# Optimization experiments

Measured on AMD Instinct MI355X. Metric: run time of the kernel, lower is better.

## Reference

```python
import jax, jax.numpy as jnp
import numpy as np

N_HEADS = 32
N_KV_HEADS = 8
HEAD_DIM = 128
ROPE_THETA = 10000.0


def _rope(x, position_ids):
    # x: [B, n_heads, T, hd], position_ids: [B, T]
    hd = x.shape[-1]
    inv_freq = 1.0 / (ROPE_THETA ** (jnp.arange(0, hd, 2, dtype=jnp.float32) / hd))  # [hd/2]
    ang = position_ids.astype(jnp.float32)[:, :, None] * inv_freq[None, None, :]  # [B, T, hd/2]
    emb = jnp.concatenate([ang, ang], axis=-1)  # [B, T, hd] (HF layout)
    cos = jnp.cos(emb)[:, None, :, :]
    sin = jnp.sin(emb)[:, None, :, :]
    x1, x2 = x[..., : hd // 2], x[..., hd // 2 :]
    rot = jnp.concatenate([-x2, x1], axis=-1)
    return x * cos + rot * sin


def setup_inputs() -> dict:
    key = jax.random.key(0)
    ks = jax.random.split(key, 9)
    B, T, D = 16, 1, 4096
    PAST = 4095
    S = PAST + T
    w = 0.02
    return {
        "hidden_states": jax.random.normal(ks[0], (B, T, D), jnp.float32),
        "attention_mask": jnp.zeros((B, 1, T, S), jnp.float32),  # additive mask, all visible
        "position_ids": jnp.full((B, T), PAST, dtype=jnp.int64),
        "past_key": jax.random.normal(ks[1], (B, N_KV_HEADS, PAST, HEAD_DIM), jnp.float32),
        "past_value": jax.random.normal(ks[2], (B, N_KV_HEADS, PAST, HEAD_DIM), jnp.float32),
        "Wq": jax.random.normal(ks[3], (N_HEADS * HEAD_DIM, D), jnp.float32) * w,
        "Wk": jax.random.normal(ks[4], (N_KV_HEADS * HEAD_DIM, D), jnp.float32) * w,
        "Wv": jax.random.normal(ks[5], (N_KV_HEADS * HEAD_DIM, D), jnp.float32) * w,
        "Wo": jax.random.normal(ks[6], (D, N_HEADS * HEAD_DIM), jnp.float32) * w,
    }


def reference(hidden_states, attention_mask, position_ids, past_key, past_value, Wq, Wk, Wv, Wo):
    B, T, D = hidden_states.shape
    hd = HEAD_DIM
    # q/k/v projections (Llama: no bias)
    q = jnp.einsum("btd,ed->bte", hidden_states, Wq).reshape(B, T, N_HEADS, hd).transpose(0, 2, 1, 3)
    k_new = jnp.einsum("btd,ed->bte", hidden_states, Wk).reshape(B, T, N_KV_HEADS, hd).transpose(0, 2, 1, 3)
    v_new = jnp.einsum("btd,ed->bte", hidden_states, Wv).reshape(B, T, N_KV_HEADS, hd).transpose(0, 2, 1, 3)
    # RoPE on the new token(s); past cache entries are already rotated
    q = _rope(q, position_ids)
    k_new = _rope(k_new, position_ids)
    # static-cache update: write new K/V at position past_seq_len (append)
    k_cache = jnp.concatenate([past_key, k_new], axis=2)   # [B, n_kv, S, hd]
    v_cache = jnp.concatenate([past_value, v_new], axis=2)
    # GQA: repeat kv heads
    n_rep = N_HEADS // N_KV_HEADS
    k = jnp.repeat(k_cache, n_rep, axis=1)  # [B, H, S, hd]
    v = jnp.repeat(v_cache, n_rep, axis=1)
    scores = jnp.einsum("bhtd,bhsd->bhts", q, k) / jnp.sqrt(jnp.float32(hd))
    scores = scores + attention_mask  # additive mask [B,1,T,S]
    w_attn = jax.nn.softmax(scores, axis=-1)
    ctx = jnp.einsum("bhts,bhsd->bhtd", w_attn, v)  # [B, H, T, hd]
    ctx = ctx.transpose(0, 2, 1, 3).reshape(B, T, N_HEADS * hd)
    attn_output = jnp.einsum("bte,de->btd", ctx, Wo)
    return attn_output, k_cache, v_cache
```

## Files before the change

### kernel.cpp

```cpp
#include <hip/hip_runtime.h>

#define NB 16
#define DMODEL 4096
#define NH 32
#define NKV 8
#define HD 128
#define SEQ 4096
#define PASTN 4095
#define EQKV 6144
#define NCHUNK 16
#define CHUNKS 256
#define PSTRIDE 136
#define SCALE 0.08838834764831845f

typedef float v4f __attribute__((ext_vector_type(4)));

__global__ __launch_bounds__(256) void qkv_proj(
    const float* __restrict__ hs, const float* __restrict__ Wq,
    const float* __restrict__ Wk, const float* __restrict__ Wv,
    float* __restrict__ raw ) {
  __shared__ __align__(16) float smem[4 * 32 * 33];
  const int tid = threadIdx.x, wid = tid >> 6, lane = tid & 63;
  const int e0 = blockIdx.x * 8 + wid * 2;

  const float* wrow[2];
#pragma unroll
  for (int r = 0; r < 2; ++r) {
    int e = e0 + r;
    wrow[r] = (e < 4096) ? (Wq + (size_t)e * DMODEL)
            : (e < 5120) ? (Wk + (size_t)(e - 4096) * DMODEL)
                         : (Wv + (size_t)(e - 5120) * DMODEL);
  }

  float acc[2][16];
#pragma unroll
  for (int r = 0; r < 2; ++r)
#pragma unroll
    for (int b = 0; b < 16; ++b) acc[r][b] = 0.f;

  float* ld = smem;
  for (int k0 = 0; k0 < DMODEL; k0 += 256) {
    __syncthreads();
#pragma unroll
    for (int i = 0; i < 4; ++i) {
      int flat = i * 1024 + tid * 4;
      int bb = flat >> 8, c = flat & 255;
      *(v4f*)(&ld[bb * 256 + c]) = *(const v4f*)(hs + (size_t)bb * DMODEL + k0 + c);
    }
    __syncthreads();
    v4f w4[2];
#pragma unroll
    for (int r = 0; r < 2; ++r) w4[r] = *(const v4f*)(wrow[r] + k0 + lane * 4);
#pragma unroll
    for (int b = 0; b < 16; ++b) {
      v4f h4 = *(const v4f*)(&ld[b * 256 + lane * 4]);
#pragma unroll
      for (int r = 0; r < 2; ++r) {
        v4f t = w4[r] * h4;
        acc[r][b] += t[0] + t[1] + t[2] + t[3];
      }
    }
  }

#pragma unroll
  for (int r = 0; r < 2; ++r)
#pragma unroll
    for (int b = 0; b < 16; ++b) acc[r][b] += __shfl_xor(acc[r][b], 32);

  __syncthreads();
  if (lane < 32) {
#pragma unroll
    for (int r = 0; r < 2; ++r)
#pragma unroll
      for (int b = 0; b < 16; ++b)
        smem[(wid * 32 + lane) * 33 + r * 16 + b] = acc[r][b];
  }
  __syncthreads();
  if (lane < 32) {
    float s = 0.f;
#pragma unroll
    for (int t2 = 0; t2 < 32; ++t2) s += smem[(wid * 32 + t2) * 33 + lane];
    const int r = lane >> 4, bb = lane & 15;
    raw[(size_t)bb * EQKV + e0 + r] = s;
  }
}

__device__ __forceinline__ float rope_val(const float* src, int d, float pos) {
  int i = d & 63;
  float inv_freq = powf(10000.f, -(float)(2 * i) * (1.f / 128.f));
  float ang = pos * inv_freq;
  float s, c;
  sincosf(ang, &s, &c);
  float x = src[d];
  float rot = (d < 64) ? -src[d + 64] : src[d - 64];
  return x * c + rot * s;
}

__global__ void rope_scatter(const float* __restrict__ raw,
                             const void* __restrict__ pos_ids,
                             float* __restrict__ qout,
                             float* __restrict__ kc, float* __restrict__ vc) {
  const int b = blockIdx.y, j = blockIdx.x, d = threadIdx.x;
  const int* pi = (const int*)pos_ids;
  long long pos = (pi[1] == 0 && pi[0] != 0) ? ((const long long*)pos_ids)[b]
                                             : (long long)pi[b];
  const float fpos = (float)pos;
  if (j < 32) {
    const float* src = raw + (size_t)b * EQKV + j * HD;
    qout[(size_t)b * (NH * HD) + j * HD + d] = rope_val(src, d, fpos);
  } else if (j < 40) {
    int kvh = j - 32;
    const float* src = raw + (size_t)b * EQKV + 4096 + kvh * HD;
    kc[(((size_t)b * NKV + kvh) * SEQ + PASTN) * HD + d] = rope_val(src, d, fpos);
  } else {
    int kvh = j - 40;
    vc[(((size_t)b * NKV + kvh) * SEQ + PASTN) * HD + d] =
        raw[(size_t)b * EQKV + 5120 + kvh * HD + d];
  }
}

__global__ __launch_bounds__(256, 4) void attn_decode(
    const float* __restrict__ pastK, const float* __restrict__ pastV,
    const float* __restrict__ qv, const float* __restrict__ mask,
    float* __restrict__ kc, float* __restrict__ vc,
    float* __restrict__ part ) {
  __shared__ __align__(16) float sm[4][4][132];

  const int chunk = blockIdx.x, kv = blockIdx.y, b = blockIdx.z;
  const int tid = threadIdx.x, wid = tid >> 6, lane = tid & 63;
  const int half = lane >> 5, q32 = lane & 31;
  const int fo = q32 * 4;

  v4f q[4];
  const float* qb = qv + (size_t)b * (NH * HD) + kv * 4 * HD + fo;
#pragma unroll
  for (int h = 0; h < 4; ++h) q[h] = *(const v4f*)(qb + h * HD);

  const size_t prow = ((size_t)b * NKV + kv) * PASTN;
  const size_t crow = ((size_t)b * NKV + kv) * SEQ;
  const int base = chunk * CHUNKS + wid * (CHUNKS / 4);
  const float* mrow = mask + (size_t)b * SEQ;

  const float mreg = mrow[base + 2 * q32 + half];

  float m[4], l[4];
  v4f c[4];
#pragma unroll
  for (int h = 0; h < 4; ++h) {
    m[h] = -1e30f; l[h] = 0.f;
    c[h] = (v4f){0.f, 0.f, 0.f, 0.f};
  }

  v4f kq[4], vq[4];
#pragma unroll
  for (int i = 0; i < 4; ++i) {
    const int s = base + 2 * i + half;
    const float* kp = (s < PASTN) ? pastK + (prow + s) * HD + fo
                                  : kc + (crow + s) * HD + fo;
    const float* vp = (s < PASTN) ? pastV + (prow + s) * HD + fo
                                  : vc + (crow + s) * HD + fo;
    kq[i] = __builtin_nontemporal_load((const v4f*)kp);
    vq[i] = __builtin_nontemporal_load((const v4f*)vp);
  }

#pragma unroll 4
  for (int t = 0; t < 32; ++t) {
    const int sp = base + 2 * t;
    const int s = sp + half;
    const v4f kch = kq[t & 3], vch = vq[t & 3];
    if (t < 28) {
      const int s2 = sp + 8 + half;
      const float* kp = (s2 < PASTN) ? pastK + (prow + s2) * HD + fo
                                     : kc + (crow + s2) * HD + fo;
      const float* vp = (s2 < PASTN) ? pastV + (prow + s2) * HD + fo
                                     : vc + (crow + s2) * HD + fo;
      kq[t & 3] = __builtin_nontemporal_load((const v4f*)kp);
      vq[t & 3] = __builtin_nontemporal_load((const v4f*)vp);
    }
    if (s < PASTN) {
      __builtin_nontemporal_store(kch, (v4f*)(kc + (crow + s) * HD + fo));
      __builtin_nontemporal_store(vch, (v4f*)(vc + (crow + s) * HD + fo));
    }

    const float mval = __shfl(mreg, t | (lane & 32));

    float d4[4];
#pragma unroll
    for (int h = 0; h < 4; ++h) {
      v4f tv = q[h] * kch;
      d4[h] = tv[0] + tv[1] + tv[2] + tv[3];
    }
#pragma unroll
    for (int off = 1; off <= 16; off <<= 1)
#pragma unroll
      for (int h = 0; h < 4; ++h) d4[h] += __shfl_xor(d4[h], off);

#pragma unroll
    for (int h = 0; h < 4; ++h) {
      float sc = d4[h] * SCALE + mval;
      if (sc > m[h]) {
        float alpha = __expf(m[h] - sc);
        l[h] *= alpha;
        c[h] *= alpha;
        m[h] = sc;
      }
      float p = __expf(sc - m[h]);
      l[h] += p;
      c[h] += p * vch;
    }
  }

#pragma unroll
  for (int h = 0; h < 4; ++h) {
    float mo = __shfl_xor(m[h], 32);
    float mn = fmaxf(m[h], mo);
    float f = __expf(m[h] - mn);
    l[h] *= f;
    c[h] *= f;
    l[h] += __shfl_xor(l[h], 32);
#pragma unroll
    for (int j = 0; j < 4; ++j) c[h][j] += __shfl_xor(c[h][j], 32);
    m[h] = mn;
  }

  if (half == 0) {
#pragma unroll
    for (int h = 0; h < 4; ++h) {
      if (q32 == 0) { sm[wid][h][0] = m[h]; sm[wid][h][1] = l[h]; }
      *(v4f*)(&sm[wid][h][4 + fo]) = c[h];
    }
  }
  __syncthreads();

  float mstar = -1e30f;
#pragma unroll
  for (int sl = 0; sl < 4; ++sl) mstar = fmaxf(mstar, sm[sl][wid][0]);
  float den = 0.f;
  const int d2 = lane * 2;
  float nx = 0.f, ny = 0.f;
#pragma unroll
  for (int sl = 0; sl < 4; ++sl) {
    float w = __expf(sm[sl][wid][0] - mstar);
    den += w * sm[sl][wid][1];
    nx += w * sm[sl][wid][4 + d2];
    ny += w * sm[sl][wid][4 + d2 + 1];
  }
  float* pp = part + (((size_t)b * NH + kv * 4 + wid) * NCHUNK + chunk) * PSTRIDE;
  if (lane == 0) { pp[0] = mstar; pp[1] = den; }
  float2 nv = {nx, ny};
  *(float2*)(pp + 4 + d2) = nv;
}

__global__ void combine(const float* __restrict__ part, float* __restrict__ ctx) {
  const int bh = blockIdx.x;
  const int lane = threadIdx.x;
  const float* pp = part + (size_t)bh * NCHUNK * PSTRIDE;
  float mstar = -1e30f;
#pragma unroll
  for (int c = 0; c < NCHUNK; ++c) mstar = fmaxf(mstar, pp[c * PSTRIDE]);
  float den = 0.f, nx = 0.f, ny = 0.f;
  const int d2 = lane * 2;
#pragma unroll
  for (int c = 0; c < NCHUNK; ++c) {
    float w = __expf(pp[c * PSTRIDE] - mstar);
    den += w * pp[c * PSTRIDE + 1];
    float2 pv = *(const float2*)(pp + c * PSTRIDE + 4 + d2);
    nx += w * pv.x;
    ny += w * pv.y;
  }
  float inv = 1.0f / den;
  ctx[(size_t)bh * HD + d2] = nx * inv;
  ctx[(size_t)bh * HD + d2 + 1] = ny * inv;
}

__global__ __launch_bounds__(256) void out_proj(
    const float* __restrict__ ctx, const float* __restrict__ Wo,
    float* __restrict__ out) {
  __shared__ __align__(16) float smem[4 * 32 * 33];
  const int tid = threadIdx.x, wid = tid >> 6, lane = tid & 63;
  const int e0 = blockIdx.x * 8 + wid * 2;

  float acc[2][16];
#pragma unroll
  for (int r = 0; r < 2; ++r)
#pragma unroll
    for (int b = 0; b < 16; ++b) acc[r][b] = 0.f;

  float* ld = smem;
  for (int k0 = 0; k0 < DMODEL; k0 += 256) {
    __syncthreads();
#pragma unroll
    for (int i = 0; i < 4; ++i) {
      int flat = i * 1024 + tid * 4;
      int bb = flat >> 8, c = flat & 255;
      *(v4f*)(&ld[bb * 256 + c]) = *(const v4f*)(ctx + (size_t)bb * DMODEL + k0 + c);
    }
    __syncthreads();
    v4f w4[2];
#pragma unroll
    for (int r = 0; r < 2; ++r)
      w4[r] = *(const v4f*)(Wo + (size_t)(e0 + r) * DMODEL + k0 + lane * 4);
#pragma unroll
    for (int b = 0; b < 16; ++b) {
      v4f h4 = *(const v4f*)(&ld[b * 256 + lane * 4]);
#pragma unroll
      for (int r = 0; r < 2; ++r) {
        v4f t = w4[r] * h4;
        acc[r][b] += t[0] + t[1] + t[2] + t[3];
      }
    }
  }

#pragma unroll
  for (int r = 0; r < 2; ++r)
#pragma unroll
    for (int b = 0; b < 16; ++b) acc[r][b] += __shfl_xor(acc[r][b], 32);

  __syncthreads();
  if (lane < 32) {
#pragma unroll
    for (int r = 0; r < 2; ++r)
#pragma unroll
      for (int b = 0; b < 16; ++b)
        smem[(wid * 32 + lane) * 33 + r * 16 + b] = acc[r][b];
  }
  __syncthreads();
  if (lane < 32) {
    float s = 0.f;
#pragma unroll
    for (int t2 = 0; t2 < 32; ++t2) s += smem[(wid * 32 + t2) * 33 + lane];
    const int r = lane >> 4, bb = lane & 15;
    out[(size_t)bb * DMODEL + e0 + r] = s;
  }
}

extern "C" void kernel_launch(void* const* d_in, const int* in_sizes, int n_in,
                              void* d_out, int out_size, void* d_ws, size_t ws_size,
                              hipStream_t stream) {
  const float* hs    = (const float*)d_in[0];
  const float* mask  = (const float*)d_in[1];
  const void*  pos   = d_in[2];
  const float* pastK = (const float*)d_in[3];
  const float* pastV = (const float*)d_in[4];
  const float* Wq    = (const float*)d_in[5];
  const float* Wk    = (const float*)d_in[6];
  const float* Wv    = (const float*)d_in[7];
  const float* Wo    = (const float*)d_in[8];

  float* out  = (float*)d_out;
  float* attn = out;
  float* kc   = out + (size_t)NB * DMODEL;
  float* vc   = kc + (size_t)NB * NKV * SEQ * HD;

  float* ws      = (float*)d_ws;
  float* ws_q    = ws;
  float* ws_raw  = ws_q + (size_t)NB * NH * HD;
  float* ws_part = ws_raw + (size_t)NB * EQKV;
  float* ws_ctx  = ws_part + (size_t)NB * NH * NCHUNK * PSTRIDE;

  qkv_proj<<<EQKV / 8, 256, 0, stream>>>(hs, Wq, Wk, Wv, ws_raw);
  rope_scatter<<<dim3(48, NB), 128, 0, stream>>>(ws_raw, pos, ws_q, kc, vc);
  attn_decode<<<dim3(NCHUNK, NKV, NB), 256, 0, stream>>>(pastK, pastV, ws_q, mask,
                                                         kc, vc, ws_part);
  combine<<<NB * NH, 64, 0, stream>>>(ws_part, ws_ctx);
  out_proj<<<DMODEL / 8, 256, 0, stream>>>(ws_ctx, Wo, attn);
}
```

Before: 289.4 us.

## Double-buffer activation and weight loads in QKV and output projection GEMVs

Both projection kernels now use two LDS buffers for the activation tile. The next chunk's activations and weight vectors are prefetched into registers while the current chunk is being computed. This gives one barrier per iteration instead of two and hides global-load latency behind the FMA work. The cost is more LDS per block (32KB plus the reduction buffer) and more registers, which may reduce occupancy.

```diff
diff --git a/kernel.cpp b/kernel.cpp
--- a/kernel.cpp
+++ b/kernel.cpp
@@ -19,9 +19,11 @@
     const float* __restrict__ hs, const float* __restrict__ Wq,
     const float* __restrict__ Wk, const float* __restrict__ Wv,
     float* __restrict__ raw ) {
-  __shared__ __align__(16) float smem[4 * 32 * 33];
+  __shared__ __align__(16) float ld[2][16][256];
+  __shared__ __align__(16) float red[4][32][33];
   const int tid = threadIdx.x, wid = tid >> 6, lane = tid & 63;
   const int e0 = blockIdx.x * 8 + wid * 2;
+  const int fo = lane * 4;
 
   const float* wrow[2];
 #pragma unroll
@@ -38,28 +40,46 @@
 #pragma unroll
     for (int b = 0; b < 16; ++b) acc[r][b] = 0.f;
 
-  float* ld = smem;
-  for (int k0 = 0; k0 < DMODEL; k0 += 256) {
-    __syncthreads();
-#pragma unroll
-    for (int i = 0; i < 4; ++i) {
-      int flat = i * 1024 + tid * 4;
-      int bb = flat >> 8, c = flat & 255;
-      *(v4f*)(&ld[bb * 256 + c]) = *(const v4f*)(hs + (size_t)bb * DMODEL + k0 + c);
-    }
-    __syncthreads();
-    v4f w4[2];
-#pragma unroll
-    for (int r = 0; r < 2; ++r) w4[r] = *(const v4f*)(wrow[r] + k0 + lane * 4);
+  v4f st[4];
+#pragma unroll
+  for (int i = 0; i < 4; ++i)
+    st[i] = *(const v4f*)(hs + (size_t)(i * 4 + wid) * DMODEL + fo);
+#pragma unroll
+  for (int i = 0; i < 4; ++i)
+    *(v4f*)(&ld[0][i * 4 + wid][fo]) = st[i];
+  v4f w4[2];
+#pragma unroll
+  for (int r = 0; r < 2; ++r) w4[r] = *(const v4f*)(wrow[r] + fo);
+  __syncthreads();
+
+  for (int c = 0; c < 16; ++c) {
+    const int k1 = (c + 1) * 256;
+    v4f w4n[2];
+    if (c < 15) {
+#pragma unroll
+      for (int i = 0; i < 4; ++i)
+        st[i] = *(const v4f*)(hs + (size_t)(i * 4 + wid) * DMODEL + k1 + fo);
+#pragma unroll
+      for (int r = 0; r < 2; ++r) w4n[r] = *(const v4f*)(wrow[r] + k1 + fo);
+    }
+    const float* lb = &ld[c & 1][0][0];
 #pragma unroll
     for (int b = 0; b < 16; ++b) {
-      v4f h4 = *(const v4f*)(&ld[b * 256 + lane * 4]);
+      v4f h4 = *(const v4f*)(lb + b * 256 + fo);
 #pragma unroll
       for (int r = 0; r < 2; ++r) {
         v4f t = w4[r] * h4;
         acc[r][b] += t[0] + t[1] + t[2] + t[3];
       }
     }
+    if (c < 15) {
+#pragma unroll
+      for (int i = 0; i < 4; ++i)
+        *(v4f*)(&ld[(c + 1) & 1][i * 4 + wid][fo]) = st[i];
+      w4[0] = w4n[0];
+      w4[1] = w4n[1];
+    }
+    __syncthreads();
   }
 
 #pragma unroll
@@ -67,19 +87,18 @@
 #pragma unroll
     for (int b = 0; b < 16; ++b) acc[r][b] += __shfl_xor(acc[r][b], 32);
 
-  __syncthreads();
   if (lane < 32) {
 #pragma unroll
     for (int r = 0; r < 2; ++r)
 #pragma unroll
       for (int b = 0; b < 16; ++b)
-        smem[(wid * 32 + lane) * 33 + r * 16 + b] = acc[r][b];
+        red[wid][lane][r * 16 + b] = acc[r][b];
   }
   __syncthreads();
   if (lane < 32) {
     float s = 0.f;
 #pragma unroll
-    for (int t2 = 0; t2 < 32; ++t2) s += smem[(wid * 32 + t2) * 33 + lane];
+    for (int t2 = 0; t2 < 32; ++t2) s += red[wid][t2][lane];
     const int r = lane >> 4, bb = lane & 15;
     raw[(size_t)bb * EQKV + e0 + r] = s;
   }
@@ -276,9 +295,11 @@
 __global__ __launch_bounds__(256) void out_proj(
     const float* __restrict__ ctx, const float* __restrict__ Wo,
     float* __restrict__ out) {
-  __shared__ __align__(16) float smem[4 * 32 * 33];
+  __shared__ __align__(16) float ld[2][16][256];
+  __shared__ __align__(16) float red[4][32][33];
   const int tid = threadIdx.x, wid = tid >> 6, lane = tid & 63;
   const int e0 = blockIdx.x * 8 + wid * 2;
+  const int fo = lane * 4;
 
   float acc[2][16];
 #pragma unroll
@@ -286,29 +307,48 @@
 #pragma unroll
     for (int b = 0; b < 16; ++b) acc[r][b] = 0.f;
 
-  float* ld = smem;
-  for (int k0 = 0; k0 < DMODEL; k0 += 256) {
-    __syncthreads();
-#pragma unroll
-    for (int i = 0; i < 4; ++i) {
-      int flat = i * 1024 + tid * 4;
-      int bb = flat >> 8, c = flat & 255;
-      *(v4f*)(&ld[bb * 256 + c]) = *(const v4f*)(ctx + (size_t)bb * DMODEL + k0 + c);
-    }
-    __syncthreads();
-    v4f w4[2];
-#pragma unroll
-    for (int r = 0; r < 2; ++r)
-      w4[r] = *(const v4f*)(Wo + (size_t)(e0 + r) * DMODEL + k0 + lane * 4);
+  v4f st[4];
+#pragma unroll
+  for (int i = 0; i < 4; ++i)
+    st[i] = *(const v4f*)(ctx + (size_t)(i * 4 + wid) * DMODEL + fo);
+#pragma unroll
+  for (int i = 0; i < 4; ++i)
+    *(v4f*)(&ld[0][i * 4 + wid][fo]) = st[i];
+  v4f w4[2];
+#pragma unroll
+  for (int r = 0; r < 2; ++r)
+    w4[r] = *(const v4f*)(Wo + (size_t)(e0 + r) * DMODEL + fo);
+  __syncthreads();
+
+  for (int c = 0; c < 16; ++c) {
+    const int k1 = (c + 1) * 256;
+    v4f w4n[2];
+    if (c < 15) {
+#pragma unroll
+      for (int i = 0; i < 4; ++i)
+        st[i] = *(const v4f*)(ctx + (size_t)(i * 4 + wid) * DMODEL + k1 + fo);
+#pragma unroll
+      for (int r = 0; r < 2; ++r)
+        w4n[r] = *(const v4f*)(Wo + (size_t)(e0 + r) * DMODEL + k1 + fo);
+    }
+    const float* lb = &ld[c & 1][0][0];
 #pragma unroll
     for (int b = 0; b < 16; ++b) {
-      v4f h4 = *(const v4f*)(&ld[b * 256 + lane * 4]);
+      v4f h4 = *(const v4f*)(lb + b * 256 + fo);
 #pragma unroll
       for (int r = 0; r < 2; ++r) {
         v4f t = w4[r] * h4;
         acc[r][b] += t[0] + t[1] + t[2] + t[3];
       }
     }
+    if (c < 15) {
+#pragma unroll
+      for (int i = 0; i < 4; ++i)
+        *(v4f*)(&ld[(c + 1) & 1][i * 4 + wid][fo]) = st[i];
+      w4[0] = w4n[0];
+      w4[1] = w4n[1];
+    }
+    __syncthreads();
   }
 
 #pragma unroll
@@ -316,19 +356,18 @@
 #pragma unroll
     for (int b = 0; b < 16; ++b) acc[r][b] += __shfl_xor(acc[r][b], 32);
 
-  __syncthreads();
   if (lane < 32) {
 #pragma unroll
     for (int r = 0; r < 2; ++r)
 #pragma unroll
       for (int b = 0; b < 16; ++b)
-        smem[(wid * 32 + lane) * 33 + r * 16 + b] = acc[r][b];
+        red[wid][lane][r * 16 + b] = acc[r][b];
   }
   __syncthreads();
   if (lane < 32) {
     float s = 0.f;
 #pragma unroll
-    for (int t2 = 0; t2 < 32; ++t2) s += smem[(wid * 32 + t2) * 33 + lane];
+    for (int t2 = 0; t2 < 32; ++t2) s += red[wid][t2][lane];
     const int r = lane >> 4, bb = lane & 15;
     out[(size_t)bb * DMODEL + e0 + r] = s;
   }
```

After: 268.0 us. 7.4% less time.
